# Kernel tuning notes

Measured on AMD Instinct MI355X. Metric: run time of the kernel, lower is better.

The kernel has to match this reference:

```python
import jax, jax.numpy as jnp
import numpy as np

HARMONICS = 5


def _harmonic_basis(x):
    k = jnp.arange(1, HARMONICS + 1, dtype=x.dtype)            # [H]
    kx = x[..., None] * k                                       # [B, D, H]
    sc = jnp.stack([jnp.sin(kx), jnp.cos(kx)], axis=-1)         # [B, D, H, 2]
    sc = sc.reshape(*x.shape, 2 * HARMONICS)                    # interleaved sin/cos
    ones = jnp.ones((*x.shape, 1), dtype=x.dtype)
    return jnp.concatenate([ones, sc], axis=-1)                 # [B, D, 2H+1]


def setup_inputs() -> dict:
    key = jax.random.key(0)
    k1, k2, k3 = jax.random.split(key, 3)
    B, D, F, H = 16384, 256, 11, 256
    x = jax.random.normal(k1, (B, D), dtype=jnp.float32)
    W = jax.random.normal(k2, (D, F, H), dtype=jnp.float32) * (1.0 / np.sqrt(F))
    b = jax.random.normal(k3, (D, H), dtype=jnp.float32) * 0.01
    return {"x": x, "W": W, "b": b}


def reference(x, W, b) -> jnp.ndarray:
    # basis expansion per feature, batched small GEMM, summed over features
    basis = _harmonic_basis(x)                                  # [B, D, F]
    out = jnp.einsum('bdf,dfh->bh', basis, W)                   # sum over features fused
    out = out + jnp.sum(b, axis=0)                              # sum of per-feature biases
    return out
```

## Files before the change

### kernel.cpp

```cpp
#include <hip/hip_runtime.h>
#include <hip/hip_bf16.h>


#define BDIM 16384
#define DDIM 256
#define HOUT 256
#define NKT  80
#define BM 64
#define BN 128

typedef __bf16 bf16x8 __attribute__((ext_vector_type(8)));
typedef float floatx4 __attribute__((ext_vector_type(4)));

__device__ __forceinline__ unsigned short f2bf(float f) {
    unsigned int u = __float_as_uint(f);
    return (unsigned short)((u + 0x7FFFu + ((u >> 16) & 1u)) >> 16);
}

__device__ __forceinline__ unsigned int pkbf(float a, float b) {
    __hip_bfloat162 r = __float22bfloat162_rn(make_float2(a, b));
    return *reinterpret_cast<unsigned int*>(&r);
}

__global__ void prep_kernel(const float* __restrict__ W, const float* __restrict__ bias,
                            unsigned short* __restrict__ Wfrag, float* __restrict__ c_part) {
    const int bid = blockIdx.x;
    const int t = threadIdx.x;
    if (bid < 4 * NKT) {
        const int kt = bid >> 2;
        const int sub = bid & 3;
        const int dtile = kt / 10;
        const int f = kt - dtile * 10 + 1;
        const int d0 = dtile * 32 + sub * 8;
        const float* wsrc = W + ((size_t)d0 * 11 + f) * 256 + t;
        union { unsigned short s[8]; int4 v; } buf;
#pragma unroll
        for (int dd = 0; dd < 8; ++dd)
            buf.s[dd] = f2bf(wsrc[(size_t)dd * 11 * 256]);
        *(int4*)(Wfrag + ((size_t)kt * 256 + t) * 32 + sub * 8) = buf.v;
    } else {
        const int p = bid - 4 * NKT;
        float acc = 0.f;
#pragma unroll
        for (int dd = 0; dd < 32; ++dd) {
            const int d = p * 32 + dd;
            acc += W[(size_t)(d * 11) * 256 + t] + bias[(size_t)d * 256 + t];
        }
        c_part[p * 256 + t] = acc;
    }
}

__device__ __forceinline__ void stage_phase(const unsigned short* __restrict__ Wfrag,
                                            unsigned short* lbuf, int ph,
                                            int h0, int wave, int l15, int koff) {
#pragma unroll
    for (int s = 0; s < 4; ++s) {
        const int c = wave * 4 + s;
        const int ktl = c >> 3;
        const int f = c & 7;
        const unsigned short* g = Wfrag + (size_t)(ph * 2 + ktl) * 8192
                                + (h0 + f * 16 + l15) * 32 + koff * 8;
        __builtin_amdgcn_global_load_lds((const void*)g, (void*)(lbuf + c * 512), 16, 0, 0);
    }
}

__global__ __launch_bounds__(256, 2)
void kan_gemm(const float* __restrict__ x, const unsigned short* __restrict__ Wfrag,
              const float* __restrict__ c_part, float* __restrict__ out) {
    __shared__ unsigned short Bs[5][2 * 8 * 512];

    const int t = threadIdx.x;
    const int m0 = blockIdx.x * BM;
    const int h0 = blockIdx.y * BN;

    const int lane = t & 63;
    const int wave = t >> 6;
    const int wr = wave >> 1;
    const int wc = wave & 1;
    const int l15 = lane & 15;
    const int koff = lane >> 4;

    floatx4 acc[2][4];
#pragma unroll
    for (int i = 0; i < 2; ++i)
#pragma unroll
        for (int j = 0; j < 4; ++j)
            acc[i][j] = (floatx4){0.f, 0.f, 0.f, 0.f};

    const float* xr0 = x + (size_t)(m0 + wr * 32 + l15) * DDIM + koff * 8;

    stage_phase(Wfrag, &Bs[0][0], 0, h0, wave, l15, koff);
    stage_phase(Wfrag, &Bs[1][0], 1, h0, wave, l15, koff);
    stage_phase(Wfrag, &Bs[2][0], 2, h0, wave, l15, koff);

    float sc[16], cc[16], sp[16], cp[16], t2c[16];

#pragma unroll 1
    for (int dt = 0; dt < 8; ++dt) {
        const float4 xa0 = *(const float4*)(xr0 + dt * 32 + 0);
        const float4 xb0 = *(const float4*)(xr0 + dt * 32 + 4);
        const float4 xa1 = *(const float4*)(xr0 + 16 * DDIM + dt * 32 + 0);
        const float4 xb1 = *(const float4*)(xr0 + 16 * DDIM + dt * 32 + 4);

#pragma unroll
        for (int q = 0; q < 5; ++q) {
            {
                int pt = dt * 5 + q + 3;
                if (pt > 39) pt = 39;
                stage_phase(Wfrag, &Bs[(q + 3) % 5][0], pt, h0, wave, l15, koff);
            }

            __builtin_amdgcn_sched_barrier(0);
            asm volatile("s_waitcnt vmcnt(8)" ::: "memory");
            __builtin_amdgcn_s_barrier();
            __builtin_amdgcn_sched_barrier(0);

            if (q == 0) {
                const float xv[16] = {xa0.x, xa0.y, xa0.z, xa0.w, xb0.x, xb0.y, xb0.z, xb0.w,
                                      xa1.x, xa1.y, xa1.z, xa1.w, xb1.x, xb1.y, xb1.z, xb1.w};
#pragma unroll
                for (int g = 0; g < 16; ++g) {
                    __sincosf(xv[g], &sc[g], &cc[g]);
                    t2c[g] = cc[g] + cc[g];
                    sp[g] = 0.f;
                    cp[g] = 1.f;
                }
            }

#pragma unroll
            for (int s = 0; s < 2; ++s) {
                const float* src = s ? cc : sc;

                union { unsigned int u[4]; bf16x8 v; } a0, a1;
#pragma unroll
                for (int p = 0; p < 4; ++p) {
                    a0.u[p] = pkbf(src[2 * p], src[2 * p + 1]);
                    a1.u[p] = pkbf(src[8 + 2 * p], src[8 + 2 * p + 1]);
                }

                const unsigned short* fb = &Bs[q][(s * 8 + wc * 4) * 512 + lane * 8];
                const bf16x8 b0 = *(const bf16x8*)(fb);
                const bf16x8 b1 = *(const bf16x8*)(fb + 512);
                const bf16x8 b2 = *(const bf16x8*)(fb + 1024);
                const bf16x8 b3 = *(const bf16x8*)(fb + 1536);

                acc[0][0] = __builtin_amdgcn_mfma_f32_16x16x32_bf16(a0.v, b0, acc[0][0], 0, 0, 0);
                acc[1][0] = __builtin_amdgcn_mfma_f32_16x16x32_bf16(a1.v, b0, acc[1][0], 0, 0, 0);
                acc[0][1] = __builtin_amdgcn_mfma_f32_16x16x32_bf16(a0.v, b1, acc[0][1], 0, 0, 0);
                acc[1][1] = __builtin_amdgcn_mfma_f32_16x16x32_bf16(a1.v, b1, acc[1][1], 0, 0, 0);
                acc[0][2] = __builtin_amdgcn_mfma_f32_16x16x32_bf16(a0.v, b2, acc[0][2], 0, 0, 0);
                acc[1][2] = __builtin_amdgcn_mfma_f32_16x16x32_bf16(a1.v, b2, acc[1][2], 0, 0, 0);
                acc[0][3] = __builtin_amdgcn_mfma_f32_16x16x32_bf16(a0.v, b3, acc[0][3], 0, 0, 0);
                acc[1][3] = __builtin_amdgcn_mfma_f32_16x16x32_bf16(a1.v, b3, acc[1][3], 0, 0, 0);

                if (s == 1 && q < 4) {
#pragma unroll
                    for (int g = 0; g < 16; ++g) {
                        const float ns = t2c[g] * sc[g] - sp[g];
                        const float nc = t2c[g] * cc[g] - cp[g];
                        sp[g] = sc[g]; cp[g] = cc[g];
                        sc[g] = ns;   cc[g] = nc;
                    }
                }
            }
        }
    }

    asm volatile("s_waitcnt vmcnt(0)" ::: "memory");

    float cj[4];
#pragma unroll
    for (int j = 0; j < 4; ++j) {
        const int col = h0 + wc * 64 + j * 16 + l15;
        float s = 0.f;
#pragma unroll
        for (int q = 0; q < 8; ++q) s += c_part[q * 256 + col];
        cj[j] = s;
    }
#pragma unroll
    for (int i = 0; i < 2; ++i) {
        const int row0 = m0 + wr * 32 + i * 16 + koff * 4;
#pragma unroll
        for (int j = 0; j < 4; ++j) {
            const int col = h0 + wc * 64 + j * 16 + l15;
#pragma unroll
            for (int r = 0; r < 4; ++r)
                out[(size_t)(row0 + r) * HOUT + col] = acc[i][j][r] + cj[j];
        }
    }
}

extern "C" void kernel_launch(void* const* d_in, const int* in_sizes, int n_in,
                              void* d_out, int out_size, void* d_ws, size_t ws_size,
                              hipStream_t stream) {
    const float* x = (const float*)d_in[0];
    const float* W = (const float*)d_in[1];
    const float* b = (const float*)d_in[2];
    float* out = (float*)d_out;

    unsigned short* Wfrag = (unsigned short*)d_ws;
    float* c_part = (float*)((char*)d_ws + (size_t)NKT * 256 * 32 * 2);

    prep_kernel<<<4 * NKT + 8, 256, 0, stream>>>(W, b, Wfrag, c_part);
    kan_gemm<<<dim3(BDIM / BM, HOUT / BN), 256, 0, stream>>>(x, Wfrag, c_part, out);
}
```

Before: 107.1 us.

## Give each wave a private LDS ring for W tiles and drop block barriers

Each wave now stages only its own 64-column slice of the W fragments into a private 5-slot LDS ring, one k-tile at a time, synchronising only with s_waitcnt and no longer with a workgroup barrier. The x row loads for the next d-tile are also issued early, mid-loop, so they overlap with the MFMAs. This removes cross-wave barrier stalls, but the two waves sharing a column half now load duplicate W data, which raises global/L2 traffic, and correctness relies on the vmcnt ordering of global_load_lds within each wave.

Measured after the change: 119.0 us. 1.11x slower.

```diff
diff --git a/kernel.cpp b/kernel.cpp
--- a/kernel.cpp
+++ b/kernel.cpp
@@ -50,24 +50,10 @@
     }
 }
 
-__device__ __forceinline__ void stage_phase(const unsigned short* __restrict__ Wfrag,
-                                            unsigned short* lbuf, int ph,
-                                            int h0, int wave, int l15, int koff) {
-#pragma unroll
-    for (int s = 0; s < 4; ++s) {
-        const int c = wave * 4 + s;
-        const int ktl = c >> 3;
-        const int f = c & 7;
-        const unsigned short* g = Wfrag + (size_t)(ph * 2 + ktl) * 8192
-                                + (h0 + f * 16 + l15) * 32 + koff * 8;
-        __builtin_amdgcn_global_load_lds((const void*)g, (void*)(lbuf + c * 512), 16, 0, 0);
-    }
-}
-
 __global__ __launch_bounds__(256, 2)
 void kan_gemm(const float* __restrict__ x, const unsigned short* __restrict__ Wfrag,
               const float* __restrict__ c_part, float* __restrict__ out) {
-    __shared__ unsigned short Bs[5][2 * 8 * 512];
+    __shared__ unsigned short Bs[4][5][2048];
 
     const int t = threadIdx.x;
     const int m0 = blockIdx.x * BM;
@@ -89,78 +75,95 @@
 
     const float* xr0 = x + (size_t)(m0 + wr * 32 + l15) * DDIM + koff * 8;
 
-    stage_phase(Wfrag, &Bs[0][0], 0, h0, wave, l15, koff);
-    stage_phase(Wfrag, &Bs[1][0], 1, h0, wave, l15, koff);
-    stage_phase(Wfrag, &Bs[2][0], 2, h0, wave, l15, koff);
+    const unsigned short* bb = Wfrag + (size_t)(h0 + wc * 64 + l15) * 32 + koff * 8;
+    unsigned short* ring = &Bs[wave][0][0];
+
+    float4 xn[4];
+    xn[0] = *(const float4*)(xr0 + 0);
+    xn[1] = *(const float4*)(xr0 + 4);
+    xn[2] = *(const float4*)(xr0 + 16 * DDIM + 0);
+    xn[3] = *(const float4*)(xr0 + 16 * DDIM + 4);
+
+#pragma unroll
+    for (int p = 0; p < 4; ++p)
+#pragma unroll
+        for (int j = 0; j < 4; ++j)
+            __builtin_amdgcn_global_load_lds((const void*)(bb + (size_t)p * 8192 + j * 512),
+                                             (void*)(ring + p * 2048 + j * 512), 16, 0, 0);
 
     float sc[16], cc[16], sp[16], cp[16], t2c[16];
 
 #pragma unroll 1
     for (int dt = 0; dt < 8; ++dt) {
-        const float4 xa0 = *(const float4*)(xr0 + dt * 32 + 0);
-        const float4 xb0 = *(const float4*)(xr0 + dt * 32 + 4);
-        const float4 xa1 = *(const float4*)(xr0 + 16 * DDIM + dt * 32 + 0);
-        const float4 xb1 = *(const float4*)(xr0 + 16 * DDIM + dt * 32 + 4);
-
-#pragma unroll
-        for (int q = 0; q < 5; ++q) {
+        {
+            const float xv[16] = {xn[0].x, xn[0].y, xn[0].z, xn[0].w,
+                                  xn[1].x, xn[1].y, xn[1].z, xn[1].w,
+                                  xn[2].x, xn[2].y, xn[2].z, xn[2].w,
+                                  xn[3].x, xn[3].y, xn[3].z, xn[3].w};
+#pragma unroll
+            for (int g = 0; g < 16; ++g) {
+                __sincosf(xv[g], &sc[g], &cc[g]);
+                t2c[g] = cc[g] + cc[g];
+                sp[g] = 0.f;
+                cp[g] = 1.f;
+            }
+        }
+
+#pragma unroll
+        for (int k5 = 0; k5 < 10; ++k5) {
+            const int slot = k5 % 5;
+            const int wslot = (k5 + 4) % 5;
+
             {
-                int pt = dt * 5 + q + 3;
-                if (pt > 39) pt = 39;
-                stage_phase(Wfrag, &Bs[(q + 3) % 5][0], pt, h0, wave, l15, koff);
-            }
-
+                int kt2 = dt * 10 + k5 + 4;
+                if (kt2 > 79) kt2 = 79;
+#pragma unroll
+                for (int j = 0; j < 4; ++j)
+                    __builtin_amdgcn_global_load_lds(
+                        (const void*)(bb + (size_t)kt2 * 8192 + j * 512),
+                        (void*)(ring + wslot * 2048 + j * 512), 16, 0, 0);
+            }
+
+            if (k5 == 5 && dt < 7) {
+                xn[0] = *(const float4*)(xr0 + (dt + 1) * 32 + 0);
+                xn[1] = *(const float4*)(xr0 + (dt + 1) * 32 + 4);
+                xn[2] = *(const float4*)(xr0 + 16 * DDIM + (dt + 1) * 32 + 0);
+                xn[3] = *(const float4*)(xr0 + 16 * DDIM + (dt + 1) * 32 + 4);
+            }
+
+            asm volatile("s_waitcnt vmcnt(16)" ::: "memory");
             __builtin_amdgcn_sched_barrier(0);
-            asm volatile("s_waitcnt vmcnt(8)" ::: "memory");
-            __builtin_amdgcn_s_barrier();
-            __builtin_amdgcn_sched_barrier(0);
-
-            if (q == 0) {
-                const float xv[16] = {xa0.x, xa0.y, xa0.z, xa0.w, xb0.x, xb0.y, xb0.z, xb0.w,
-                                      xa1.x, xa1.y, xa1.z, xa1.w, xb1.x, xb1.y, xb1.z, xb1.w};
+
+            const float* src = (k5 & 1) ? cc : sc;
+            union { unsigned int u[4]; bf16x8 v; } a0, a1;
+#pragma unroll
+            for (int p = 0; p < 4; ++p) {
+                a0.u[p] = pkbf(src[2 * p], src[2 * p + 1]);
+                a1.u[p] = pkbf(src[8 + 2 * p], src[8 + 2 * p + 1]);
+            }
+
+            const unsigned short* fb = ring + slot * 2048 + lane * 8;
+            const bf16x8 b0 = *(const bf16x8*)(fb);
+            const bf16x8 b1 = *(const bf16x8*)(fb + 512);
+            const bf16x8 b2 = *(const bf16x8*)(fb + 1024);
+            const bf16x8 b3 = *(const bf16x8*)(fb + 1536);
+
+            acc[0][0] = __builtin_amdgcn_mfma_f32_16x16x32_bf16(a0.v, b0, acc[0][0], 0, 0, 0);
+            acc[1][0] = __builtin_amdgcn_mfma_f32_16x16x32_bf16(a1.v, b0, acc[1][0], 0, 0, 0);
+            acc[0][1] = __builtin_amdgcn_mfma_f32_16x16x32_bf16(a0.v, b1, acc[0][1], 0, 0, 0);
+            acc[1][1] = __builtin_amdgcn_mfma_f32_16x16x32_bf16(a1.v, b1, acc[1][1], 0, 0, 0);
+            acc[0][2] = __builtin_amdgcn_mfma_f32_16x16x32_bf16(a0.v, b2, acc[0][2], 0, 0, 0);
+            acc[1][2] = __builtin_amdgcn_mfma_f32_16x16x32_bf16(a1.v, b2, acc[1][2], 0, 0, 0);
+            acc[0][3] = __builtin_amdgcn_mfma_f32_16x16x32_bf16(a0.v, b3, acc[0][3], 0, 0, 0);
+            acc[1][3] = __builtin_amdgcn_mfma_f32_16x16x32_bf16(a1.v, b3, acc[1][3], 0, 0, 0);
+
+            if ((k5 & 1) && k5 < 9) {
 #pragma unroll
                 for (int g = 0; g < 16; ++g) {
-                    __sincosf(xv[g], &sc[g], &cc[g]);
-                    t2c[g] = cc[g] + cc[g];
-                    sp[g] = 0.f;
-                    cp[g] = 1.f;
-                }
-            }
-
-#pragma unroll
-            for (int s = 0; s < 2; ++s) {
-                const float* src = s ? cc : sc;
-
-                union { unsigned int u[4]; bf16x8 v; } a0, a1;
-#pragma unroll
-                for (int p = 0; p < 4; ++p) {
-                    a0.u[p] = pkbf(src[2 * p], src[2 * p + 1]);
-                    a1.u[p] = pkbf(src[8 + 2 * p], src[8 + 2 * p + 1]);
-                }
-
-                const unsigned short* fb = &Bs[q][(s * 8 + wc * 4) * 512 + lane * 8];
-                const bf16x8 b0 = *(const bf16x8*)(fb);
-                const bf16x8 b1 = *(const bf16x8*)(fb + 512);
-                const bf16x8 b2 = *(const bf16x8*)(fb + 1024);
-                const bf16x8 b3 = *(const bf16x8*)(fb + 1536);
-
-                acc[0][0] = __builtin_amdgcn_mfma_f32_16x16x32_bf16(a0.v, b0, acc[0][0], 0, 0, 0);
-                acc[1][0] = __builtin_amdgcn_mfma_f32_16x16x32_bf16(a1.v, b0, acc[1][0], 0, 0, 0);
-                acc[0][1] = __builtin_amdgcn_mfma_f32_16x16x32_bf16(a0.v, b1, acc[0][1], 0, 0, 0);
-                acc[1][1] = __builtin_amdgcn_mfma_f32_16x16x32_bf16(a1.v, b1, acc[1][1], 0, 0, 0);
-                acc[0][2] = __builtin_amdgcn_mfma_f32_16x16x32_bf16(a0.v, b2, acc[0][2], 0, 0, 0);
-                acc[1][2] = __builtin_amdgcn_mfma_f32_16x16x32_bf16(a1.v, b2, acc[1][2], 0, 0, 0);
-                acc[0][3] = __builtin_amdgcn_mfma_f32_16x16x32_bf16(a0.v, b3, acc[0][3], 0, 0, 0);
-                acc[1][3] = __builtin_amdgcn_mfma_f32_16x16x32_bf16(a1.v, b3, acc[1][3], 0, 0, 0);
-
-                if (s == 1 && q < 4) {
-#pragma unroll
-                    for (int g = 0; g < 16; ++g) {
-                        const float ns = t2c[g] * sc[g] - sp[g];
-                        const float nc = t2c[g] * cc[g] - cp[g];
-                        sp[g] = sc[g]; cp[g] = cc[g];
-                        sc[g] = ns;   cc[g] = nc;
-                    }
+                    const float ns = t2c[g] * sc[g] - sp[g];
+                    const float nc = t2c[g] * cc[g] - cp[g];
+                    sp[g] = sc[g]; cp[g] = cc[g];
+                    sc[g] = ns;   cc[g] = nc;
                 }
             }
         }
```

## Double M tile to 128 rows with 8 waves and prefetch next x slice

Applied to the files above, without the earlier changes.

The batch tile grows from 64 to 128 rows and each block now runs 512 threads (8 waves), so each staged W fragment in LDS is shared by twice as many rows. Each wave now stages 2 chunks per phase instead of 4. The x values for the next d-tile are loaded early, at q==2, so their latency overlaps the MFMA work, and the vmcnt waits are adjusted to account for those extra loads. The added waves per CU under launch bounds (512,2) shrink the per-thread register budget, which risks spills given the many live sin/cos recurrence arrays.

Measured after the change: 102.4 us. 4.4% less time.

```diff
diff --git a/kernel.cpp b/kernel.cpp
--- a/kernel.cpp
+++ b/kernel.cpp
@@ -6,7 +6,7 @@
 #define DDIM 256
 #define HOUT 256
 #define NKT  80
-#define BM 64
+#define BM 128
 #define BN 128
 
 typedef __bf16 bf16x8 __attribute__((ext_vector_type(8)));
@@ -50,24 +50,10 @@
     }
 }
 
-__device__ __forceinline__ void stage_phase(const unsigned short* __restrict__ Wfrag,
-                                            unsigned short* lbuf, int ph,
-                                            int h0, int wave, int l15, int koff) {
-#pragma unroll
-    for (int s = 0; s < 4; ++s) {
-        const int c = wave * 4 + s;
-        const int ktl = c >> 3;
-        const int f = c & 7;
-        const unsigned short* g = Wfrag + (size_t)(ph * 2 + ktl) * 8192
-                                + (h0 + f * 16 + l15) * 32 + koff * 8;
-        __builtin_amdgcn_global_load_lds((const void*)g, (void*)(lbuf + c * 512), 16, 0, 0);
-    }
-}
-
-__global__ __launch_bounds__(256, 2)
+__global__ __launch_bounds__(512, 2)
 void kan_gemm(const float* __restrict__ x, const unsigned short* __restrict__ Wfrag,
               const float* __restrict__ c_part, float* __restrict__ out) {
-    __shared__ unsigned short Bs[5][2 * 8 * 512];
+    __shared__ unsigned short Bs[6][2 * 8 * 512];
 
     const int t = threadIdx.x;
     const int m0 = blockIdx.x * BM;
@@ -89,35 +75,72 @@
 
     const float* xr0 = x + (size_t)(m0 + wr * 32 + l15) * DDIM + koff * 8;
 
-    stage_phase(Wfrag, &Bs[0][0], 0, h0, wave, l15, koff);
-    stage_phase(Wfrag, &Bs[1][0], 1, h0, wave, l15, koff);
-    stage_phase(Wfrag, &Bs[2][0], 2, h0, wave, l15, koff);
+    const unsigned short* bb = Wfrag + (size_t)(h0 + l15 * 1) * 0 + 0;
+
+    float4 xn[4];
+    xn[0] = *(const float4*)(xr0 + 0);
+    xn[1] = *(const float4*)(xr0 + 4);
+    xn[2] = *(const float4*)(xr0 + 16 * DDIM + 0);
+    xn[3] = *(const float4*)(xr0 + 16 * DDIM + 4);
+
+#pragma unroll
+    for (int p = 0; p < 3; ++p) {
+#pragma unroll
+        for (int s = 0; s < 2; ++s) {
+            const int c = wave * 2 + s;
+            const int ktl = c >> 3;
+            const int f = c & 7;
+            const unsigned short* g = Wfrag + (size_t)(p * 2 + ktl) * 8192
+                                    + (h0 + f * 16 + l15) * 32 + koff * 8;
+            __builtin_amdgcn_global_load_lds((const void*)g,
+                (void*)(&Bs[p][0] + c * 512), 16, 0, 0);
+        }
+    }
 
     float sc[16], cc[16], sp[16], cp[16], t2c[16];
 
 #pragma unroll 1
     for (int dt = 0; dt < 8; ++dt) {
-        const float4 xa0 = *(const float4*)(xr0 + dt * 32 + 0);
-        const float4 xb0 = *(const float4*)(xr0 + dt * 32 + 4);
-        const float4 xa1 = *(const float4*)(xr0 + 16 * DDIM + dt * 32 + 0);
-        const float4 xb1 = *(const float4*)(xr0 + 16 * DDIM + dt * 32 + 4);
-
 #pragma unroll
         for (int q = 0; q < 5; ++q) {
+
+            if (q == 2) {
+                const int dn = (dt < 7) ? dt + 1 : 7;
+                xn[0] = *(const float4*)(xr0 + dn * 32 + 0);
+                xn[1] = *(const float4*)(xr0 + dn * 32 + 4);
+                xn[2] = *(const float4*)(xr0 + 16 * DDIM + dn * 32 + 0);
+                xn[3] = *(const float4*)(xr0 + 16 * DDIM + dn * 32 + 4);
+            }
+
             {
                 int pt = dt * 5 + q + 3;
                 if (pt > 39) pt = 39;
-                stage_phase(Wfrag, &Bs[(q + 3) % 5][0], pt, h0, wave, l15, koff);
+#pragma unroll
+                for (int s = 0; s < 2; ++s) {
+                    const int c = wave * 2 + s;
+                    const int ktl = c >> 3;
+                    const int f = c & 7;
+                    const unsigned short* g = Wfrag + (size_t)(pt * 2 + ktl) * 8192
+                                            + (h0 + f * 16 + l15) * 32 + koff * 8;
+                    __builtin_amdgcn_global_load_lds((const void*)g,
+                        (void*)(&Bs[(q + 3) % 5][0] + c * 512), 16, 0, 0);
+                }
             }
 
             __builtin_amdgcn_sched_barrier(0);
-            asm volatile("s_waitcnt vmcnt(8)" ::: "memory");
+            if (q == 2 || q == 3) {
+                asm volatile("s_waitcnt vmcnt(10)" ::: "memory");
+            } else {
+                asm volatile("s_waitcnt vmcnt(6)" ::: "memory");
+            }
             __builtin_amdgcn_s_barrier();
             __builtin_amdgcn_sched_barrier(0);
 
             if (q == 0) {
-                const float xv[16] = {xa0.x, xa0.y, xa0.z, xa0.w, xb0.x, xb0.y, xb0.z, xb0.w,
-                                      xa1.x, xa1.y, xa1.z, xa1.w, xb1.x, xb1.y, xb1.z, xb1.w};
+                const float xv[16] = {xn[0].x, xn[0].y, xn[0].z, xn[0].w,
+                                      xn[1].x, xn[1].y, xn[1].z, xn[1].w,
+                                      xn[2].x, xn[2].y, xn[2].z, xn[2].w,
+                                      xn[3].x, xn[3].y, xn[3].z, xn[3].w};
 #pragma unroll
                 for (int g = 0; g < 16; ++g) {
                     __sincosf(xv[g], &sc[g], &cc[g]);
@@ -202,5 +225,5 @@
     float* c_part = (float*)((char*)d_ws + (size_t)NKT * 256 * 32 * 2);
 
     prep_kernel<<<4 * NKT + 8, 256, 0, stream>>>(W, b, Wfrag, c_part);
-    kan_gemm<<<dim3(BDIM / BM, HOUT / BN), 256, 0, stream>>>(x, Wfrag, c_part, out);
-}
+    kan_gemm<<<dim3(BDIM / BM, HOUT / BN), 512, 0, stream>>>(x, Wfrag, c_part, out);
+}
```
